# Kernel optimization log

Measured on AMD Instinct MI355X. Metric: run time of the kernel, lower is better.

## Reference

```python
import jax, jax.numpy as jnp
import numpy as np
from jax import lax

L, T, DM, DH = 4, 4096, 2048, 1024
MAX_PHASE = 6.28
EPS = 1e-5


def setup_inputs() -> dict:
    key = jax.random.key(0)
    ks = jax.random.split(key, 16)
    # LRU initializers (r_min=0, r_max=1)
    u1 = jax.random.uniform(ks[0], (L, DH))
    nu_log = jnp.log(-0.5 * jnp.log(u1))
    u2 = jax.random.uniform(ks[1], (L, DH))
    theta_log = jnp.log(MAX_PHASE * u2)
    abs_lam = jnp.exp(-jnp.exp(nu_log))  # |lambda|
    gamma_log = jnp.log(jnp.sqrt(1.0 - abs_lam ** 2))
    B_re = jax.random.normal(ks[2], (L, DH, DM)) / np.sqrt(2 * DM)
    B_im = jax.random.normal(ks[3], (L, DH, DM)) / np.sqrt(2 * DM)
    C_re = jax.random.normal(ks[4], (L, DM, DH)) / np.sqrt(DH)
    C_im = jax.random.normal(ks[5], (L, DM, DH)) / np.sqrt(DH)
    D = jax.random.normal(ks[6], (L, DM))
    bound = 1.0 / np.sqrt(DM)
    enc_w = jax.random.uniform(ks[7], (DM, DM), minval=-bound, maxval=bound)
    enc_b = jax.random.uniform(ks[8], (DM,), minval=-bound, maxval=bound)
    out1_w = jax.random.uniform(ks[9], (L, DM, DM), minval=-bound, maxval=bound)
    out1_b = jax.random.uniform(ks[10], (L, DM), minval=-bound, maxval=bound)
    out2_w = jax.random.uniform(ks[11], (L, DM, DM), minval=-bound, maxval=bound)
    out2_b = jax.random.uniform(ks[12], (L, DM), minval=-bound, maxval=bound)
    norm_w = jnp.ones((L, DM))
    norm_b = jnp.zeros((L, DM))
    x = jax.random.normal(ks[13], (T, DM))
    return dict(x=x, enc_w=enc_w, enc_b=enc_b, nu_log=nu_log, theta_log=theta_log,
                gamma_log=gamma_log, B_re=B_re, B_im=B_im, C_re=C_re, C_im=C_im,
                D=D, norm_w=norm_w, norm_b=norm_b, out1_w=out1_w, out1_b=out1_b,
                out2_w=out2_w, out2_b=out2_b)


def _lru(xn, nu, th, gl, br, bi, cr, ci, d):
    # xn: (T, DM) real -> (T, DM) real
    lam = jnp.exp(-jnp.exp(nu) + 1j * jnp.exp(th))          # (DH,) complex
    B_norm = (br + 1j * bi) * jnp.exp(gl)[:, None]           # (DH, DM)
    Bu = xn.astype(B_norm.dtype) @ B_norm.T                  # (T, DH) complex
    a = jnp.broadcast_to(lam, Bu.shape)
    def combine(e1, e2):
        a1, b1 = e1
        a2, b2 = e2
        return a1 * a2, a2 * b1 + b2
    _, h = lax.associative_scan(combine, (a, Bu), axis=0)    # h_t = lam*h_{t-1} + Bu_t
    C = cr + 1j * ci
    return (h @ C.T).real + xn * d


def _batchnorm(x, w, b):
    # training-mode BatchNorm1d over dim 0 (biased variance), matching torch
    mu = x.mean(axis=0)
    var = jnp.mean((x - mu) ** 2, axis=0)
    return (x - mu) / jnp.sqrt(var + EPS) * w + b


def _forward(x, enc_w, enc_b, nu_log, theta_log, gamma_log, B_re, B_im,
             C_re, C_im, D, norm_w, norm_b, out1_w, out1_b, out2_w, out2_b):
    x = x @ enc_w.T + enc_b
    def layer(carry, p):
        nu, th, gl, br, bi, cr, ci, d, nw, nb, w1, b1, w2, b2 = p
        xn = _batchnorm(carry, nw, nb)
        y = _lru(xn, nu, th, gl, br, bi, cr, ci, d)
        y = jax.nn.gelu(y, approximate=False)
        y = (y @ w1.T + b1) * jax.nn.sigmoid(y @ w2.T + b2)
        return carry + y, None
    x, _ = lax.scan(layer, x, (nu_log, theta_log, gamma_log, B_re, B_im,
                               C_re, C_im, D, norm_w, norm_b,
                               out1_w, out1_b, out2_w, out2_b))
    return x


def reference(x, enc_w, enc_b, nu_log, theta_log, gamma_log, B_re, B_im,
              C_re, C_im, D, norm_w, norm_b, out1_w, out1_b, out2_w, out2_b):
    return _forward(x, enc_w, enc_b, nu_log, theta_log, gamma_log, B_re, B_im,
                    C_re, C_im, D, norm_w, norm_b, out1_w, out1_b, out2_w, out2_b)
```

## Files before the change

### kernel.cpp

```cpp
#include <hip/hip_runtime.h>
#include <stdint.h>
#include <math.h>


#define LAYERS 4
#define TT     4096
#define DMODEL 2048
#define DHID   1024
#define NCHUNK 64
#define CLEN   64
#define KTILES 64

typedef unsigned short ushort_t;
typedef __attribute__((ext_vector_type(8))) _Float16 half8;
typedef __attribute__((ext_vector_type(4))) float    f32x4;

__device__ __forceinline__ unsigned pack2h(float a, float b) {
  _Float16 ha = (_Float16)a, hb = (_Float16)b;
  unsigned short ua = *(unsigned short*)&ha, ub = *(unsigned short*)&hb;
  return (unsigned)ua | ((unsigned)ub << 16);
}

__device__ __forceinline__ void get_lam(const float* nu_log, const float* th_log,
                                        int h, float& lre, float& lim)
{
  const float mag = expf(-expf(nu_log[h]));
  const float th  = expf(th_log[h]);
  lre = mag * cosf(th);
  lim = mag * sinf(th);
}

__global__ __launch_bounds__(256)
void convert_h(const float* __restrict__ B0, const float* __restrict__ B1,
               int ldb, int NS, int KS, ushort_t* __restrict__ Hi)
{
  __shared__ float tile[128][33];
  const int mb  = blockIdx.x;
  const int kb  = blockIdx.y;
  const int tid = threadIdx.x;
  const int r0  = tid >> 3;
  const int c0  = (tid & 7) * 4;
#pragma unroll
  for (int rep = 0; rep < 4; ++rep) {
    const int rr = rep * 32 + r0;
    const int n  = mb * 128 + rr;
    const int k  = kb * 32 + c0;
    const float* bp; long idx;
    if (n >= NS)      { bp = B1; idx = (long)(n - NS) * ldb + k; }
    else if (k >= KS) { bp = B1; idx = (long)n * ldb + (k - KS); }
    else              { bp = B0; idx = (long)n * ldb + k; }
#pragma unroll
    for (int u = 0; u < 4; ++u) tile[rr][c0 + u] = bp[idx + u];
  }
  __syncthreads();
#pragma unroll
  for (int rep = 0; rep < 2; ++rep) {
    const int id2 = rep * 256 + tid;
    const int kg  = id2 >> 7;
    const int m   = id2 & 127;
    const long off = ((long)mb * KTILES + kb) * 4096 + (kg * 128 + m) * 8;
    unsigned hw[4];
#pragma unroll
    for (int p = 0; p < 4; ++p)
      hw[p] = pack2h(tile[m][kg * 8 + p * 2], tile[m][kg * 8 + p * 2 + 1]);
    *(uint4*)&Hi[off] = make_uint4(hw[0], hw[1], hw[2], hw[3]);
  }
}

__global__ __launch_bounds__(256)
void convert_ilv_rows(const float* __restrict__ P0, const float* __restrict__ P1,
                      int ldb, ushort_t* __restrict__ Hi)
{
  __shared__ float tile[128][33];
  const int mb  = blockIdx.x;
  const int kb  = blockIdx.y;
  const int tid = threadIdx.x;
  const int r0  = tid >> 3;
  const int c0  = (tid & 7) * 4;
#pragma unroll
  for (int rep = 0; rep < 4; ++rep) {
    const int rr = rep * 32 + r0;
    const int n  = mb * 128 + rr;
    const float* bp = (n & 1) ? P1 : P0;
    const long idx = (long)(n >> 1) * ldb + kb * 32 + c0;
#pragma unroll
    for (int u = 0; u < 4; ++u) tile[rr][c0 + u] = bp[idx + u];
  }
  __syncthreads();
#pragma unroll
  for (int rep = 0; rep < 2; ++rep) {
    const int id2 = rep * 256 + tid;
    const int kg  = id2 >> 7;
    const int m   = id2 & 127;
    const long off = ((long)mb * KTILES + kb) * 4096 + (kg * 128 + m) * 8;
    unsigned hw[4];
#pragma unroll
    for (int p = 0; p < 4; ++p)
      hw[p] = pack2h(tile[m][kg * 8 + p * 2], tile[m][kg * 8 + p * 2 + 1]);
    *(uint4*)&Hi[off] = make_uint4(hw[0], hw[1], hw[2], hw[3]);
  }
}

__global__ __launch_bounds__(256)
void convert_ilv_cols(const float* __restrict__ P0, const float* __restrict__ P1,
                      int ldb, ushort_t* __restrict__ Hi)
{
  __shared__ float tile[128][33];
  const int mb  = blockIdx.x;
  const int kb  = blockIdx.y;
  const int tid = threadIdx.x;
  const int r0  = tid >> 3;
  const int c0  = (tid & 7) * 4;
#pragma unroll
  for (int rep = 0; rep < 4; ++rep) {
    const int rr = rep * 32 + r0;
    const int n  = mb * 128 + rr;
    const long base = (long)n * ldb + ((kb * 32 + c0) >> 1);
    tile[rr][c0 + 0] = P0[base];
    tile[rr][c0 + 1] = P1[base];
    tile[rr][c0 + 2] = P0[base + 1];
    tile[rr][c0 + 3] = P1[base + 1];
  }
  __syncthreads();
#pragma unroll
  for (int rep = 0; rep < 2; ++rep) {
    const int id2 = rep * 256 + tid;
    const int kg  = id2 >> 7;
    const int m   = id2 & 127;
    const long off = ((long)mb * KTILES + kb) * 4096 + (kg * 128 + m) * 8;
    unsigned hw[4];
#pragma unroll
    for (int p = 0; p < 4; ++p)
      hw[p] = pack2h(tile[m][kg * 8 + p * 2], tile[m][kg * 8 + p * 2 + 1]);
    *(uint4*)&Hi[off] = make_uint4(hw[0], hw[1], hw[2], hw[3]);
  }
}

__global__ __launch_bounds__(256)
void bn_convert(const float* __restrict__ carry, const float* __restrict__ stats,
                const float* __restrict__ nw, const float* __restrict__ nb,
                ushort_t* __restrict__ Hi)
{
  __shared__ float tile[128][33];
  const int mb  = blockIdx.x;
  const int kb  = blockIdx.y;
  const int tid = threadIdx.x;
  const int r0  = tid >> 3;
  const int c0  = (tid & 7) * 4;
  float mean[4], rstd[4], w_[4], b_[4];
#pragma unroll
  for (int u = 0; u < 4; ++u) {
    const int j = kb * 32 + c0 + u;
    const float mu = stats[j] * (1.0f / TT);
    const float va = fmaxf(stats[DMODEL + j] * (1.0f / TT) - mu * mu, 0.0f);
    mean[u] = mu; rstd[u] = rsqrtf(va + 1e-5f);
    w_[u] = nw[j]; b_[u] = nb[j];
  }
#pragma unroll
  for (int rep = 0; rep < 4; ++rep) {
    const int rr  = rep * 32 + r0;
    const long base = (long)(mb * 128 + rr) * 2048 + kb * 32 + c0;
#pragma unroll
    for (int u = 0; u < 4; ++u)
      tile[rr][c0 + u] = (carry[base + u] - mean[u]) * rstd[u] * w_[u] + b_[u];
  }
  __syncthreads();
#pragma unroll
  for (int rep = 0; rep < 2; ++rep) {
    const int id2 = rep * 256 + tid;
    const int kg  = id2 >> 7;
    const int m   = id2 & 127;
    const long off = ((long)mb * KTILES + kb) * 4096 + (kg * 128 + m) * 8;
    unsigned hw[4];
#pragma unroll
    for (int p = 0; p < 4; ++p)
      hw[p] = pack2h(tile[m][kg * 8 + p * 2], tile[m][kg * 8 + p * 2 + 1]);
    *(uint4*)&Hi[off] = make_uint4(hw[0], hw[1], hw[2], hw[3]);
  }
}

__global__ __launch_bounds__(256)
void scan3_convert(const float* __restrict__ loc,
                   const float* __restrict__ ccre, const float* __restrict__ ccim,
                   const float* __restrict__ nu_log, const float* __restrict__ th_log,
                   ushort_t* __restrict__ Hi)
{
  __shared__ float tile[128][33];
  const int mb  = blockIdx.x;
  const int kb  = blockIdx.y;
  const int tid = threadIdx.x;
  const int r0  = tid >> 3;
  const int c0  = (tid & 7) * 4;
  float en[4], eth[4], cr0[4], ci0[4], cr1[4], ci1[4];
  int   im[4];
#pragma unroll
  for (int u = 0; u < 4; ++u) {
    const int col = kb * 32 + c0 + u;
    const int h   = col >> 1;
    im[u]  = col & 1;
    en[u]  = expf(nu_log[h]);
    eth[u] = expf(th_log[h]);
    cr0[u] = ccre[(mb * 2) * DHID + h];     ci0[u] = ccim[(mb * 2) * DHID + h];
    cr1[u] = ccre[(mb * 2 + 1) * DHID + h]; ci1[u] = ccim[(mb * 2 + 1) * DHID + h];
  }
#pragma unroll
  for (int rep = 0; rep < 4; ++rep) {
    const int rr  = rep * 32 + r0;
    const int sel = rr >> 6;
    const float p = (float)((rr & 63) + 1);
    const long base = (long)(mb * 128 + rr) * 2048 + kb * 32 + c0;
#pragma unroll
    for (int u = 0; u < 4; ++u) {
      const float magp = expf(-p * en[u]);
      const float ang  = p * eth[u];
      float sv, cv;
      __sincosf(ang, &sv, &cv);
      const float pr = magp * cv, pi = magp * sv;
      const float cr_ = sel ? cr1[u] : cr0[u];
      const float ci_ = sel ? ci1[u] : ci0[u];
      const float L = loc[base + u];
      tile[rr][c0 + u] = im[u] ? -(L + pr * ci_ + pi * cr_)
                               :  (L + pr * cr_ - pi * ci_);
    }
  }
  __syncthreads();
#pragma unroll
  for (int rep = 0; rep < 2; ++rep) {
    const int id2 = rep * 256 + tid;
    const int kg  = id2 >> 7;
    const int m   = id2 & 127;
    const long off = ((long)mb * KTILES + kb) * 4096 + (kg * 128 + m) * 8;
    unsigned hw[4];
#pragma unroll
    for (int p2 = 0; p2 < 4; ++p2)
      hw[p2] = pack2h(tile[m][kg * 8 + p2 * 2], tile[m][kg * 8 + p2 * 2 + 1]);
    *(uint4*)&Hi[off] = make_uint4(hw[0], hw[1], hw[2], hw[3]);
  }
}

#define GLDS(gp, lp) __builtin_amdgcn_global_load_lds( \
    (__attribute__((address_space(1))) void*)(void*)(gp), \
    (__attribute__((address_space(3))) void*)(lp), 16, 0, 0)

__global__ __launch_bounds__(256, 4)
void gemm_mfma(const ushort_t* __restrict__ Ahi, const ushort_t* __restrict__ Bhi,
               float* __restrict__ C, const float* __restrict__ bias,
               int epi, float* __restrict__ stats,
               ushort_t* __restrict__ gT,
               const float* __restrict__ dvec,
               const float* __restrict__ nu_log, const float* __restrict__ th_log,
               const float* __restrict__ gl_log)
{
  __shared__ ushort_t S[2][8192];
  const int tid  = threadIdx.x;
  const int lane = tid & 63;
  const int wid  = tid >> 6;
  const int wm   = wid >> 1;
  const int wn   = wid & 1;

  const int bid = blockIdx.y * gridDim.x + blockIdx.x;
  const int xcd = bid & 7, idx = bid >> 3;
  const int mb  = ((xcd & 3) << 3) | (idx & 7);
  const int nb  = ((xcd >> 2) << 3) | (idx >> 3);

  f32x4 acc[4][4];
#pragma unroll
  for (int i = 0; i < 4; ++i)
#pragma unroll
    for (int j = 0; j < 4; ++j) acc[i][j] = (f32x4){0.f, 0.f, 0.f, 0.f};

  const ushort_t* ga = Ahi + (long)mb * KTILES * 4096 + tid * 8;
  const ushort_t* gb = Bhi + (long)nb * KTILES * 4096 + tid * 8;

  const int albase = ((lane >> 4) * 128 + wm * 64 + (lane & 15)) * 8;
  const int blbase = ((lane >> 4) * 128 + wn * 64 + (lane & 15)) * 8;

  half8 Af[4], Bf[4];

#define STAGE(P) \
  GLDS(ga,        &S[P][tid * 8]); \
  GLDS(ga + 2048, &S[P][2048 + tid * 8]); \
  GLDS(gb,        &S[P][4096 + tid * 8]); \
  GLDS(gb + 2048, &S[P][6144 + tid * 8]); \
  ga += 4096; gb += 4096;

#define RD(P) \
  _Pragma("unroll") \
  for (int m = 0; m < 4; ++m) Af[m] = *(const half8*)&S[P][albase + m * 128]; \
  _Pragma("unroll") \
  for (int n = 0; n < 4; ++n) Bf[n] = *(const half8*)&S[P][4096 + blbase + n * 128];

#define MFMA16 \
  __builtin_amdgcn_s_setprio(1); \
  _Pragma("unroll") \
  for (int m = 0; m < 4; ++m) \
    _Pragma("unroll") \
    for (int n = 0; n < 4; ++n) \
      acc[m][n] = __builtin_amdgcn_mfma_f32_16x16x32_f16(Af[m], Bf[n], acc[m][n], 0, 0, 0); \
  __builtin_amdgcn_s_setprio(0);

#define WAIT_VM_BAR(n) asm volatile("s_waitcnt vmcnt(" #n ")" ::: "memory"); \
  __builtin_amdgcn_sched_barrier(0); __builtin_amdgcn_s_barrier();
#define LGKM0_BAR asm volatile("s_waitcnt lgkmcnt(0)" ::: "memory"); \
  __builtin_amdgcn_sched_barrier(0); __builtin_amdgcn_s_barrier();

#define KSTEP(P) \
  WAIT_VM_BAR(4) \
  RD(P) \
  MFMA16 \
  LGKM0_BAR \
  STAGE(P)

  STAGE(0)
  STAGE(1)
  for (int it = 0; it < 31; ++it) {
    KSTEP(0)
    KSTEP(1)
  }
  WAIT_VM_BAR(4)
  RD(0)
  MFMA16
  WAIT_VM_BAR(0)
  RD(1)
  MFMA16
#undef STAGE
#undef RD
#undef MFMA16
#undef WAIT_VM_BAR
#undef LGKM0_BAR
#undef KSTEP

  const int cn = lane & 15;
  const int cr = (lane >> 4) * 4;

  if (epi == 0) {
    float s0[4] = {0.f, 0.f, 0.f, 0.f}, s1[4] = {0.f, 0.f, 0.f, 0.f};
#pragma unroll
    for (int m = 0; m < 4; ++m) {
      const long row = (long)mb * 128 + wm * 64 + m * 16 + cr;
#pragma unroll
      for (int n = 0; n < 4; ++n) {
        const int col = nb * 128 + wn * 64 + n * 16 + cn;
        const float bv = bias ? bias[col] : 0.0f;
#pragma unroll
        for (int q = 0; q < 4; ++q) {
          const float v = acc[m][n][q] + bv;
          C[(row + q) * 2048 + col] = v;
          s0[n] += v; s1[n] += v * v;
        }
      }
    }
    if (stats) {
      __syncthreads();
      float* sred = (float*)&S[0][0];
      if (tid < 256) sred[tid] = 0.f;
      __syncthreads();
#pragma unroll
      for (int n = 0; n < 4; ++n) {
        const int lc = wn * 64 + n * 16 + cn;
        atomicAdd(&sred[lc], s0[n]);
        atomicAdd(&sred[128 + lc], s1[n]);
      }
      __syncthreads();
      if (tid < 128) {
        atomicAdd(&stats[nb * 128 + tid], sred[tid]);
        atomicAdd(&stats[DMODEL + nb * 128 + tid], sred[128 + tid]);
      }
    }
    return;
  }

  float* Lf = (float*)&S[0][0];

  if (epi == 1) {
    float gamma = 0.f, lre = 0.f, lim = 0.f;
    if (tid < 64) {
      const int hg = nb * 64 + tid;
      gamma = expf(gl_log[hg]);
      get_lam(nu_log, th_log, hg, lre, lim);
    }
#pragma unroll
    for (int half = 0; half < 2; ++half) {
      __syncthreads();
      if (wm == half) {
#pragma unroll
        for (int m = 0; m < 4; ++m)
#pragma unroll
          for (int n = 0; n < 4; ++n)
#pragma unroll
            for (int q = 0; q < 4; ++q)
              Lf[(m * 16 + cr + q) * 128 + wn * 64 + n * 16 + cn] = acc[m][n][q];
      }
      __syncthreads();
      if (tid < 64) {
        const int p = tid;
        float hr = 0.f, hi = 0.f;
        const long base = ((long)mb * 128 + half * 64) * 2048 + nb * 128 + 2 * p;
        for (int i = 0; i < 64; ++i) {
          const float br_ = Lf[i * 128 + 2 * p]     * gamma;
          const float bi_ = Lf[i * 128 + 2 * p + 1] * gamma;
          const float nr = lre * hr - lim * hi + br_;
          const float ni = lre * hi + lim * hr + bi_;
          hr = nr; hi = ni;
          *(float2*)&C[base + (long)i * 2048] = make_float2(hr, hi);
        }
      }
    }
    return;
  }

  {
#pragma unroll
    for (int half = 0; half < 2; ++half) {
      __syncthreads();
      if (wm == half) {
#pragma unroll
        for (int m = 0; m < 4; ++m)
#pragma unroll
          for (int n = 0; n < 4; ++n)
#pragma unroll
            for (int q = 0; q < 4; ++q)
              Lf[(m * 16 + cr + q) * 128 + wn * 64 + n * 16 + cn] = acc[m][n][q];
      }
      __syncthreads();
#pragma unroll
      for (int c = 0; c < 4; ++c) {
        const int chunk = c * 256 + tid;
        const int mloc = chunk & 63;
        const int kg   = (chunk >> 6) & 3;
        const int lt   = chunk >> 8;
        const int m    = half * 64 + mloc;
        const long off = ((long)mb * KTILES + nb * 4 + lt) * 4096 + (kg * 128 + m) * 8;
        const half8 xh = *(const half8*)&gT[off];
        const float* Lrow = &Lf[mloc * 128 + lt * 32 + kg * 8];
        const float* dp = dvec + nb * 128 + lt * 32 + kg * 8;
        unsigned hw[4];
#pragma unroll
        for (int p = 0; p < 4; ++p) {
          float g2[2];
#pragma unroll
          for (int e = 0; e < 2; ++e) {
            const int j = p * 2 + e;
            const float v = Lrow[j] + (float)xh[j] * dp[j];
            g2[e] = 0.5f * v * (1.0f + erff(v * 0.70710678118654752440f));
          }
          hw[p] = pack2h(g2[0], g2[1]);
        }
        *(uint4*)&gT[off] = make_uint4(hw[0], hw[1], hw[2], hw[3]);
      }
    }
  }
}

__global__ __launch_bounds__(256, 4)
void gemm_dual(const ushort_t* __restrict__ Ahi, const ushort_t* __restrict__ B1t,
               const ushort_t* __restrict__ B2t,
               float* __restrict__ carry, const float* __restrict__ b1,
               const float* __restrict__ b2, float* __restrict__ stats)
{
  __shared__ ushort_t S[2][8192];
  const int tid  = threadIdx.x;
  const int lane = tid & 63;
  const int wid  = tid >> 6;
  const int wm   = wid >> 1;
  const int wn   = wid & 1;

  const int bid = blockIdx.y * gridDim.x + blockIdx.x;
  const int xcd = bid & 7, idx = bid >> 3;
  const int mb  = ((xcd & 3) << 3) | (idx & 7);
  const int nbb = ((xcd >> 2) << 4) | (idx >> 3);

  f32x4 acc1[4][2], acc2[4][2];
#pragma unroll
  for (int i = 0; i < 4; ++i)
#pragma unroll
    for (int j = 0; j < 2; ++j) {
      acc1[i][j] = (f32x4){0.f, 0.f, 0.f, 0.f};
      acc2[i][j] = (f32x4){0.f, 0.f, 0.f, 0.f};
    }

  const int nt = nbb >> 1;
  const int hb = nbb & 1;

  const ushort_t* ga = Ahi + (long)mb * KTILES * 4096 + tid * 8;
  const long boff = ((tid >> 6) * 128 + hb * 64 + (tid & 63)) * 8;
  const ushort_t* g1 = B1t + (long)nt * KTILES * 4096 + boff;
  const ushort_t* g2 = B2t + (long)nt * KTILES * 4096 + boff;

  const int albase = ((lane >> 4) * 128 + wm * 64 + (lane & 15)) * 8;
  const int blbase = ((lane >> 4) * 64 + wn * 32 + (lane & 15)) * 8;

  half8 Af[4], B1f[2], B2f[2];

#define STAGE(P) \
  GLDS(ga,        &S[P][tid * 8]); \
  GLDS(ga + 2048, &S[P][2048 + tid * 8]); \
  GLDS(g1,        &S[P][4096 + tid * 8]); \
  GLDS(g2,        &S[P][6144 + tid * 8]); \
  ga += 4096; g1 += 4096; g2 += 4096;

#define RD(P) \
  _Pragma("unroll") \
  for (int m = 0; m < 4; ++m) Af[m]  = *(const half8*)&S[P][albase + m * 128]; \
  _Pragma("unroll") \
  for (int n = 0; n < 2; ++n) B1f[n] = *(const half8*)&S[P][4096 + blbase + n * 128]; \
  _Pragma("unroll") \
  for (int n = 0; n < 2; ++n) B2f[n] = *(const half8*)&S[P][6144 + blbase + n * 128];

#define MFMA16D \
  __builtin_amdgcn_s_setprio(1); \
  _Pragma("unroll") \
  for (int m = 0; m < 4; ++m) \
    _Pragma("unroll") \
    for (int n = 0; n < 2; ++n) \
      acc1[m][n] = __builtin_amdgcn_mfma_f32_16x16x32_f16(Af[m], B1f[n], acc1[m][n], 0, 0, 0); \
  _Pragma("unroll") \
  for (int m = 0; m < 4; ++m) \
    _Pragma("unroll") \
    for (int n = 0; n < 2; ++n) \
      acc2[m][n] = __builtin_amdgcn_mfma_f32_16x16x32_f16(Af[m], B2f[n], acc2[m][n], 0, 0, 0); \
  __builtin_amdgcn_s_setprio(0);

#define WAIT_VM_BAR(n) asm volatile("s_waitcnt vmcnt(" #n ")" ::: "memory"); \
  __builtin_amdgcn_sched_barrier(0); __builtin_amdgcn_s_barrier();
#define LGKM0_BAR asm volatile("s_waitcnt lgkmcnt(0)" ::: "memory"); \
  __builtin_amdgcn_sched_barrier(0); __builtin_amdgcn_s_barrier();

#define KSTEPD(P) \
  WAIT_VM_BAR(4) \
  RD(P) \
  MFMA16D \
  LGKM0_BAR \
  STAGE(P)

  STAGE(0)
  STAGE(1)
  for (int it = 0; it < 31; ++it) {
    KSTEPD(0)
    KSTEPD(1)
  }
  WAIT_VM_BAR(4)
  RD(0)
  MFMA16D
  WAIT_VM_BAR(0)
  RD(1)
  MFMA16D
#undef STAGE
#undef RD
#undef MFMA16D
#undef WAIT_VM_BAR
#undef LGKM0_BAR
#undef KSTEPD

  const int cn = lane & 15;
  const int cr = (lane >> 4) * 4;
  float s0[2] = {0.f, 0.f}, s1[2] = {0.f, 0.f};
#pragma unroll
  for (int m = 0; m < 4; ++m) {
    const long row = (long)mb * 128 + wm * 64 + m * 16 + cr;
#pragma unroll
    for (int n = 0; n < 2; ++n) {
      const int col = nbb * 64 + wn * 32 + n * 16 + cn;
      const float b1v = b1[col], b2v = b2[col];
#pragma unroll
      for (int q = 0; q < 4; ++q) {
        const long idx2 = (row + q) * 2048 + col;
        const float t1v = acc1[m][n][q] + b1v;
        const float t2v = acc2[m][n][q] + b2v;
        const float v = carry[idx2] + t1v * (1.0f / (1.0f + expf(-t2v)));
        carry[idx2] = v;
        s0[n] += v; s1[n] += v * v;
      }
    }
  }
  if (stats) {
    __syncthreads();
    float* sred = (float*)&S[0][0];
    if (tid < 128) sred[tid] = 0.f;
    __syncthreads();
#pragma unroll
    for (int n = 0; n < 2; ++n) {
      const int lc = wn * 32 + n * 16 + cn;
      atomicAdd(&sred[lc], s0[n]);
      atomicAdd(&sred[64 + lc], s1[n]);
    }
    __syncthreads();
    if (tid < 64) {
      atomicAdd(&stats[nbb * 64 + tid], sred[tid]);
      atomicAdd(&stats[DMODEL + nbb * 64 + tid], sred[64 + tid]);
    }
  }
}

__global__ void scan2(const float* __restrict__ loc,
                      float* __restrict__ ccre, float* __restrict__ ccim,
                      const float* __restrict__ nu_log, const float* __restrict__ th_log)
{
  const int h = blockIdx.x * 256 + threadIdx.x;
  float lre, lim; get_lam(nu_log, th_log, h, lre, lim);
  float ar = lre, ai = lim;
  for (int s = 0; s < 6; ++s) { float nr = ar * ar - ai * ai, ni = 2.f * ar * ai; ar = nr; ai = ni; }
  float er = 0.f, ei = 0.f;
  for (int c = 0; c < NCHUNK; ++c) {
    ccre[c * DHID + h] = er; ccim[c * DHID + h] = ei;
    const long t = (long)c * CLEN + (CLEN - 1);
    const float nr = ar * er - ai * ei + loc[t * 2048 + 2 * h];
    const float ni = ar * ei + ai * er + loc[t * 2048 + 2 * h + 1];
    er = nr; ei = ni;
  }
}

__global__ void finalize(const float* __restrict__ carry, float* __restrict__ out)
{
  const long idx = (long)blockIdx.x * 256 + threadIdx.x;
  const float v = carry[idx];
  out[idx] = (v == v && fabsf(v) < 3.0e38f) ? v : 300000.0f;
}

__global__ void diagfill(float* __restrict__ out, float val)
{
  const long idx = (long)blockIdx.x * 256 + threadIdx.x;
  out[idx] = (idx == 0) ? val : 0.0f;
}

extern "C" void kernel_launch(void* const* d_in, const int* in_sizes, int n_in,
                              void* d_out, int out_size, void* d_ws, size_t ws_size,
                              hipStream_t stream)
{
  (void)out_size;
  const int EW = (TT * DMODEL) / 256;
  float* out = (float*)d_out;

  if (n_in != 17 || in_sizes[0] != TT * DMODEL) {
    diagfill<<<EW, 256, 0, stream>>>(out, (float)(1 << 18));
    return;
  }
  if (ws_size < 151600000ull) {
    diagfill<<<EW, 256, 0, stream>>>(out, (float)(1 << 12));
    return;
  }

  const float* x     = (const float*)d_in[0];
  const float* enc_w = (const float*)d_in[1];
  const float* enc_b = (const float*)d_in[2];
  const float* nu    = (const float*)d_in[3];
  const float* th    = (const float*)d_in[4];
  const float* gl    = (const float*)d_in[5];
  const float* Bre   = (const float*)d_in[6];
  const float* Bim   = (const float*)d_in[7];
  const float* Cre   = (const float*)d_in[8];
  const float* Cim   = (const float*)d_in[9];
  const float* Dd    = (const float*)d_in[10];
  const float* nw    = (const float*)d_in[11];
  const float* nb    = (const float*)d_in[12];
  const float* w1    = (const float*)d_in[13];
  const float* b1    = (const float*)d_in[14];
  const float* w2    = (const float*)d_in[15];
  const float* b2    = (const float*)d_in[16];

  char* ws = (char*)d_ws;
  float*    carry = (float*)(ws);
  ushort_t* AhiX  = (ushort_t*)(ws + 33554432);
  float*    buf1  = (float*)(ws + 67108864);
  ushort_t* Ahi   = (ushort_t*)(ws + 100663296);
  ushort_t* B2hi  = (ushort_t*)(ws + 117440512);
  ushort_t* Bhi   = (ushort_t*)(ws + 134217728);
  float*    ccre  = (float*)(ws + 150994944);
  float*    ccim  = (float*)(ws + 151257088);
  float*    stats = (float*)(ws + 151519232);

  const dim3 gcA(32, 64);
  const dim3 gcW(16, 64);
  const dim3 gg(32, 16);
  const dim3 gg2(32, 32);
  const int BIG = 1 << 30;

  hipMemsetAsync(stats, 0, 2 * DMODEL * sizeof(float), stream);
  convert_h<<<gcA, 256, 0, stream>>>(x, x, 2048, BIG, BIG, Ahi);
  convert_h<<<gcW, 256, 0, stream>>>(enc_w, enc_w, 2048, BIG, BIG, Bhi);
  gemm_mfma<<<gg, 256, 0, stream>>>(Ahi, Bhi, carry, enc_b, 0, stats,
                                    nullptr, nullptr, nullptr, nullptr, nullptr);

  for (int l = 0; l < LAYERS; ++l) {
    const float* Brl = Bre + (size_t)l * DHID * DMODEL;
    const float* Bil = Bim + (size_t)l * DHID * DMODEL;
    const float* Crl = Cre + (size_t)l * DMODEL * DHID;
    const float* Cil = Cim + (size_t)l * DMODEL * DHID;
    const float* w1l = w1 + (size_t)l * DMODEL * DMODEL;
    const float* w2l = w2 + (size_t)l * DMODEL * DMODEL;

    bn_convert<<<gcA, 256, 0, stream>>>(carry, stats, nw + l * DMODEL,
                                        nb + l * DMODEL, AhiX);

    convert_ilv_rows<<<gcW, 256, 0, stream>>>(Brl, Bil, 2048, Bhi);
    gemm_mfma<<<gg, 256, 0, stream>>>(AhiX, Bhi, buf1, nullptr, 1, nullptr,
                                      nullptr, nullptr,
                                      nu + l * DHID, th + l * DHID, gl + l * DHID);

    scan2<<<4, 256, 0, stream>>>(buf1, ccre, ccim, nu + l * DHID, th + l * DHID);

    convert_ilv_cols<<<gcW, 256, 0, stream>>>(Crl, Cil, 1024, Bhi);
    scan3_convert<<<gcA, 256, 0, stream>>>(buf1, ccre, ccim, nu + l * DHID,
                                           th + l * DHID, Ahi);

    gemm_mfma<<<gg, 256, 0, stream>>>(Ahi, Bhi, nullptr, nullptr, 2, nullptr,
                                      AhiX, Dd + l * DMODEL,
                                      nullptr, nullptr, nullptr);

    convert_h<<<gcW, 256, 0, stream>>>(w1l, w1l, 2048, BIG, BIG, Bhi);
    convert_h<<<gcW, 256, 0, stream>>>(w2l, w2l, 2048, BIG, BIG, B2hi);
    float* nstats = (l < LAYERS - 1) ? stats : nullptr;
    if (nstats) hipMemsetAsync(stats, 0, 2 * DMODEL * sizeof(float), stream);
    gemm_dual<<<gg2, 256, 0, stream>>>(AhiX, Bhi, B2hi, carry,
                                       b1 + l * DMODEL, b2 + l * DMODEL, nstats);
  }

  finalize<<<EW, 256, 0, stream>>>(carry, out);
}
```

Baseline: 1.178 ms.

## Emit fp16 tiled chunk-scan output from GEMM epilogue and merge weight conversions

The epilogue of the B-projection GEMM now writes the intra-chunk scan result as fp16 directly into the tiled MFMA operand layout, plus a small fp32 buffer holding only each chunk's last state. This replaces the full fp32 (T, 2*DH) intermediate. scan2 reads only those last states, and scan3_convert reads the fp16 tiles with no LDS transpose. The two per-layer w1/w2 fp16 conversions are merged into one launch. The intent is less HBM traffic and fewer launches, at the cost of rounding the local scan states to fp16 before the carry correction is added.

```diff
diff --git a/kernel.cpp b/kernel.cpp
--- a/kernel.cpp
+++ b/kernel.cpp
@@ -68,6 +68,41 @@
 }
 
 __global__ __launch_bounds__(256)
+void convert_w12(const float* __restrict__ w1, const float* __restrict__ w2,
+                 ushort_t* __restrict__ H1, ushort_t* __restrict__ H2)
+{
+  __shared__ float tile[128][33];
+  const int mb  = blockIdx.x;
+  const int kb  = blockIdx.y;
+  const int tid = threadIdx.x;
+  const int r0  = tid >> 3;
+  const int c0  = (tid & 7) * 4;
+  const float* src = (mb < 16) ? w1 : w2;
+  ushort_t*    dst = (mb < 16) ? H1 : H2;
+  const int    mbl = mb & 15;
+#pragma unroll
+  for (int rep = 0; rep < 4; ++rep) {
+    const int rr = rep * 32 + r0;
+    const long idx = (long)(mbl * 128 + rr) * 2048 + kb * 32 + c0;
+#pragma unroll
+    for (int u = 0; u < 4; ++u) tile[rr][c0 + u] = src[idx + u];
+  }
+  __syncthreads();
+#pragma unroll
+  for (int rep = 0; rep < 2; ++rep) {
+    const int id2 = rep * 256 + tid;
+    const int kg  = id2 >> 7;
+    const int m   = id2 & 127;
+    const long off = ((long)mbl * KTILES + kb) * 4096 + (kg * 128 + m) * 8;
+    unsigned hw[4];
+#pragma unroll
+    for (int p = 0; p < 4; ++p)
+      hw[p] = pack2h(tile[m][kg * 8 + p * 2], tile[m][kg * 8 + p * 2 + 1]);
+    *(uint4*)&dst[off] = make_uint4(hw[0], hw[1], hw[2], hw[3]);
+  }
+}
+
+__global__ __launch_bounds__(256)
 void convert_ilv_rows(const float* __restrict__ P0, const float* __restrict__ P1,
                       int ldb, ushort_t* __restrict__ Hi)
 {
@@ -180,60 +215,40 @@
 }
 
 __global__ __launch_bounds__(256)
-void scan3_convert(const float* __restrict__ loc,
+void scan3_convert(const ushort_t* __restrict__ locT,
                    const float* __restrict__ ccre, const float* __restrict__ ccim,
                    const float* __restrict__ nu_log, const float* __restrict__ th_log,
                    ushort_t* __restrict__ Hi)
 {
-  __shared__ float tile[128][33];
   const int mb  = blockIdx.x;
   const int kb  = blockIdx.y;
   const int tid = threadIdx.x;
-  const int r0  = tid >> 3;
-  const int c0  = (tid & 7) * 4;
-  float en[4], eth[4], cr0[4], ci0[4], cr1[4], ci1[4];
-  int   im[4];
-#pragma unroll
-  for (int u = 0; u < 4; ++u) {
-    const int col = kb * 32 + c0 + u;
-    const int h   = col >> 1;
-    im[u]  = col & 1;
-    en[u]  = expf(nu_log[h]);
-    eth[u] = expf(th_log[h]);
-    cr0[u] = ccre[(mb * 2) * DHID + h];     ci0[u] = ccim[(mb * 2) * DHID + h];
-    cr1[u] = ccre[(mb * 2 + 1) * DHID + h]; ci1[u] = ccim[(mb * 2 + 1) * DHID + h];
-  }
-#pragma unroll
-  for (int rep = 0; rep < 4; ++rep) {
-    const int rr  = rep * 32 + r0;
-    const int sel = rr >> 6;
-    const float p = (float)((rr & 63) + 1);
-    const long base = (long)(mb * 128 + rr) * 2048 + kb * 32 + c0;
-#pragma unroll
-    for (int u = 0; u < 4; ++u) {
-      const float magp = expf(-p * en[u]);
-      const float ang  = p * eth[u];
+#pragma unroll
+  for (int rep = 0; rep < 2; ++rep) {
+    const int chunk = rep * 256 + tid;
+    const int kg = chunk >> 7;
+    const int m  = chunk & 127;
+    const long off = ((long)mb * KTILES + kb) * 4096 + (kg * 128 + m) * 8;
+    const half8 L = *(const half8*)&locT[off];
+    const int   ch = mb * 2 + (m >> 6);
+    const float p  = (float)((m & 63) + 1);
+    unsigned hw[4];
+#pragma unroll
+    for (int jp = 0; jp < 4; ++jp) {
+      const int col = kb * 32 + kg * 8 + 2 * jp;
+      const int h   = col >> 1;
+      const float en  = expf(nu_log[h]);
+      const float eth = expf(th_log[h]);
+      const float magp = expf(-p * en);
       float sv, cv;
-      __sincosf(ang, &sv, &cv);
+      __sincosf(p * eth, &sv, &cv);
       const float pr = magp * cv, pi = magp * sv;
-      const float cr_ = sel ? cr1[u] : cr0[u];
-      const float ci_ = sel ? ci1[u] : ci0[u];
-      const float L = loc[base + u];
-      tile[rr][c0 + u] = im[u] ? -(L + pr * ci_ + pi * cr_)
-                               :  (L + pr * cr_ - pi * ci_);
-    }
-  }
-  __syncthreads();
-#pragma unroll
-  for (int rep = 0; rep < 2; ++rep) {
-    const int id2 = rep * 256 + tid;
-    const int kg  = id2 >> 7;
-    const int m   = id2 & 127;
-    const long off = ((long)mb * KTILES + kb) * 4096 + (kg * 128 + m) * 8;
-    unsigned hw[4];
-#pragma unroll
-    for (int p2 = 0; p2 < 4; ++p2)
-      hw[p2] = pack2h(tile[m][kg * 8 + p2 * 2], tile[m][kg * 8 + p2 * 2 + 1]);
+      const float crv = ccre[ch * DHID + h];
+      const float civ = ccim[ch * DHID + h];
+      const float vre =  ((float)L[2 * jp]     + pr * crv - pi * civ);
+      const float vim = -((float)L[2 * jp + 1] + pr * civ + pi * crv);
+      hw[jp] = pack2h(vre, vim);
+    }
     *(uint4*)&Hi[off] = make_uint4(hw[0], hw[1], hw[2], hw[3]);
   }
 }
@@ -395,15 +410,33 @@
       if (tid < 64) {
         const int p = tid;
         float hr = 0.f, hi = 0.f;
-        const long base = ((long)mb * 128 + half * 64) * 2048 + nb * 128 + 2 * p;
         for (int i = 0; i < 64; ++i) {
           const float br_ = Lf[i * 128 + 2 * p]     * gamma;
           const float bi_ = Lf[i * 128 + 2 * p + 1] * gamma;
           const float nr = lre * hr - lim * hi + br_;
           const float ni = lre * hi + lim * hr + bi_;
           hr = nr; hi = ni;
-          *(float2*)&C[base + (long)i * 2048] = make_float2(hr, hi);
+          Lf[i * 128 + 2 * p]     = hr;
+          Lf[i * 128 + 2 * p + 1] = hi;
         }
+        C[(long)(mb * 2 + half) * 2048 + nb * 128 + 2 * p]     = hr;
+        C[(long)(mb * 2 + half) * 2048 + nb * 128 + 2 * p + 1] = hi;
+      }
+      __syncthreads();
+#pragma unroll
+      for (int c = 0; c < 4; ++c) {
+        const int chunk = c * 256 + tid;
+        const int mloc = chunk & 63;
+        const int kg   = (chunk >> 6) & 3;
+        const int lt   = chunk >> 8;
+        const int m    = half * 64 + mloc;
+        const long off = ((long)mb * KTILES + nb * 4 + lt) * 4096 + (kg * 128 + m) * 8;
+        const float* Lrow = &Lf[mloc * 128 + lt * 32 + kg * 8];
+        unsigned hw[4];
+#pragma unroll
+        for (int p2 = 0; p2 < 4; ++p2)
+          hw[p2] = pack2h(Lrow[p2 * 2], Lrow[p2 * 2 + 1]);
+        *(uint4*)&gT[off] = make_uint4(hw[0], hw[1], hw[2], hw[3]);
       }
     }
     return;
@@ -523,14 +556,13 @@
 
 #define WAIT_VM_BAR(n) asm volatile("s_waitcnt vmcnt(" #n ")" ::: "memory"); \
   __builtin_amdgcn_sched_barrier(0); __builtin_amdgcn_s_barrier();
-#define LGKM0_BAR asm volatile("s_waitcnt lgkmcnt(0)" ::: "memory"); \
-  __builtin_amdgcn_sched_barrier(0); __builtin_amdgcn_s_barrier();
 
 #define KSTEPD(P) \
   WAIT_VM_BAR(4) \
   RD(P) \
   MFMA16D \
-  LGKM0_BAR \
+  asm volatile("s_waitcnt lgkmcnt(0)" ::: "memory"); \
+  __builtin_amdgcn_sched_barrier(0); __builtin_amdgcn_s_barrier(); \
   STAGE(P)
 
   STAGE(0)
@@ -549,7 +581,6 @@
 #undef RD
 #undef MFMA16D
 #undef WAIT_VM_BAR
-#undef LGKM0_BAR
 #undef KSTEPD
 
   const int cn = lane & 15;
@@ -592,7 +623,7 @@
   }
 }
 
-__global__ void scan2(const float* __restrict__ loc,
+__global__ void scan2(const float* __restrict__ locLast,
                       float* __restrict__ ccre, float* __restrict__ ccim,
                       const float* __restrict__ nu_log, const float* __restrict__ th_log)
 {
@@ -603,9 +634,8 @@
   float er = 0.f, ei = 0.f;
   for (int c = 0; c < NCHUNK; ++c) {
     ccre[c * DHID + h] = er; ccim[c * DHID + h] = ei;
-    const long t = (long)c * CLEN + (CLEN - 1);
-    const float nr = ar * er - ai * ei + loc[t * 2048 + 2 * h];
-    const float ni = ar * ei + ai * er + loc[t * 2048 + 2 * h + 1];
+    const float nr = ar * er - ai * ei + locLast[(long)c * 2048 + 2 * h];
+    const float ni = ar * ei + ai * er + locLast[(long)c * 2048 + 2 * h + 1];
     er = nr; ei = ni;
   }
 }
@@ -659,18 +689,20 @@
   const float* b2    = (const float*)d_in[16];
 
   char* ws = (char*)d_ws;
-  float*    carry = (float*)(ws);
-  ushort_t* AhiX  = (ushort_t*)(ws + 33554432);
-  float*    buf1  = (float*)(ws + 67108864);
-  ushort_t* Ahi   = (ushort_t*)(ws + 100663296);
-  ushort_t* B2hi  = (ushort_t*)(ws + 117440512);
-  ushort_t* Bhi   = (ushort_t*)(ws + 134217728);
-  float*    ccre  = (float*)(ws + 150994944);
-  float*    ccim  = (float*)(ws + 151257088);
-  float*    stats = (float*)(ws + 151519232);
+  float*    carry   = (float*)(ws);
+  ushort_t* AhiX    = (ushort_t*)(ws + 33554432);
+  ushort_t* locT    = (ushort_t*)(ws + 67108864);
+  float*    locLast = (float*)(ws + 83886080);
+  ushort_t* Ahi     = (ushort_t*)(ws + 100663296);
+  ushort_t* B2hi    = (ushort_t*)(ws + 117440512);
+  ushort_t* Bhi     = (ushort_t*)(ws + 134217728);
+  float*    ccre    = (float*)(ws + 150994944);
+  float*    ccim    = (float*)(ws + 151257088);
+  float*    stats   = (float*)(ws + 151519232);
 
   const dim3 gcA(32, 64);
   const dim3 gcW(16, 64);
+  const dim3 gcW2(32, 64);
   const dim3 gg(32, 16);
   const dim3 gg2(32, 32);
   const int BIG = 1 << 30;
@@ -693,22 +725,21 @@
                                         nb + l * DMODEL, AhiX);
 
     convert_ilv_rows<<<gcW, 256, 0, stream>>>(Brl, Bil, 2048, Bhi);
-    gemm_mfma<<<gg, 256, 0, stream>>>(AhiX, Bhi, buf1, nullptr, 1, nullptr,
-                                      nullptr, nullptr,
+    gemm_mfma<<<gg, 256, 0, stream>>>(AhiX, Bhi, locLast, nullptr, 1, nullptr,
+                                      locT, nullptr,
                                       nu + l * DHID, th + l * DHID, gl + l * DHID);
 
-    scan2<<<4, 256, 0, stream>>>(buf1, ccre, ccim, nu + l * DHID, th + l * DHID);
+    scan2<<<4, 256, 0, stream>>>(locLast, ccre, ccim, nu + l * DHID, th + l * DHID);
 
     convert_ilv_cols<<<gcW, 256, 0, stream>>>(Crl, Cil, 1024, Bhi);
-    scan3_convert<<<gcA, 256, 0, stream>>>(buf1, ccre, ccim, nu + l * DHID,
+    scan3_convert<<<gcA, 256, 0, stream>>>(locT, ccre, ccim, nu + l * DHID,
                                            th + l * DHID, Ahi);
 
     gemm_mfma<<<gg, 256, 0, stream>>>(Ahi, Bhi, nullptr, nullptr, 2, nullptr,
                                       AhiX, Dd + l * DMODEL,
                                       nullptr, nullptr, nullptr);
 
-    convert_h<<<gcW, 256, 0, stream>>>(w1l, w1l, 2048, BIG, BIG, Bhi);
-    convert_h<<<gcW, 256, 0, stream>>>(w2l, w2l, 2048, BIG, BIG, B2hi);
+    convert_w12<<<gcW2, 256, 0, stream>>>(w1l, w2l, Bhi, B2hi);
     float* nstats = (l < LAYERS - 1) ? stats : nullptr;
     if (nstats) hipMemsetAsync(stats, 0, 2 * DMODEL * sizeof(float), stream);
     gemm_dual<<<gg2, 256, 0, stream>>>(AhiX, Bhi, B2hi, carry,
```

After: 1.165 ms. About the same (-1.1%).
